# Kernel tuning notes

Hardware: AMD Instinct MI355X
Metric: run time of the kernel (lower is better)

The kernel has to match this reference:

```python
import jax, jax.numpy as jnp
import numpy as np

B, N, D, L = 8, 128, 512, 48
NUM_GCN_LAYERS = 2


def setup_inputs() -> dict:
    key = jax.random.key(0)
    ks = jax.random.split(key, 10)
    gcn_inputs = jax.random.normal(ks[0], (B, N, D), dtype=jnp.float32)
    word_seq_len = jax.random.randint(ks[1], (B,), 1, N + 1)
    adj_matrix = jax.random.randint(ks[2], (B, N, N), 0, 2).astype(jnp.float32)
    dep_label_matrix = jax.random.randint(ks[3], (B, N, N), 0, L)
    # per-label weight matrices, stored (L, out_dim, in_dim) as consumed by the bmm
    w_params = jax.random.normal(ks[4], (L, D, D), dtype=jnp.float32) * 0.05
    mlp_w0 = jax.random.normal(ks[5], (D, D), dtype=jnp.float32) * (1.0 / np.sqrt(D))
    mlp_b0 = jnp.zeros((D,), dtype=jnp.float32)
    mlp_w1 = jax.random.normal(ks[6], (D, D), dtype=jnp.float32) * (1.0 / np.sqrt(D))
    mlp_b1 = jnp.zeros((D,), dtype=jnp.float32)
    return {
        'gcn_inputs': gcn_inputs,
        'word_seq_len': word_seq_len,
        'adj_matrix': adj_matrix,
        'dep_label_matrix': dep_label_matrix,
        'w_params': w_params,
        'mlp_w0': mlp_w0,
        'mlp_b0': mlp_b0,
        'mlp_w1': mlp_w1,
        'mlp_b1': mlp_b1,
    }


def reference(gcn_inputs, word_seq_len, adj_matrix, dep_label_matrix,
              w_params, mlp_w0, mlp_b0, mlp_w1, mlp_b1):
    # denom: in-degree + 1 (self)
    denom = adj_matrix.sum(axis=2, keepdims=True) + 1.0  # (B, N, 1)
    b_idx = jnp.arange(B)[:, None, None]                  # (B,1,1)
    j_idx = jnp.arange(N)[None, None, :]                  # (1,1,N)
    h = gcn_inputs
    for _ in range(NUM_GCN_LAYERS):
        # transform every node by every label matrix: (B, L, N, D)
        t = jnp.einsum('ldk,bjk->bljd', w_params, h)
        # gather per-edge label transform: g[b,i,j,:] = t[b, lab[b,i,j], j, :]
        g = t[b_idx, dep_label_matrix, j_idx]             # (B, N, N, D)
        msg = (adj_matrix[..., None] * g).sum(axis=2)     # (B, N, D)
        h = jax.nn.relu(msg / denom)
    x = jax.nn.relu(h @ mlp_w0.T + mlp_b0)
    x = jax.nn.relu(x @ mlp_w1.T + mlp_b1)
    return x
```

## Files before the change

kernel.cpp:

```cpp
#include <hip/hip_runtime.h>
#include <hip/hip_bf16.h>


typedef unsigned short u16;
typedef unsigned int u32;
using bf16x8 = __bf16 __attribute__((ext_vector_type(8)));
using f32x4 = float __attribute__((ext_vector_type(4)));

__device__ __forceinline__ u16 f2bf(float f) {
  u32 u = __float_as_uint(f);
  u32 r = u + 0x7fffu + ((u >> 16) & 1u);
  return (u16)(r >> 16);
}
__device__ __forceinline__ float bf2f(u16 h) {
  return __uint_as_float(((u32)h) << 16);
}

__device__ __forceinline__ void gl_lds16(const u16* g, u16* l) {
  __builtin_amdgcn_global_load_lds(
      (const __attribute__((address_space(1))) u32*)g,
      (__attribute__((address_space(3))) u32*)l, 16, 0, 0);
}

__global__ __launch_bounds__(256)
void cvt_all(const float* __restrict__ w_in, u16* __restrict__ w_out,
             const float* __restrict__ h_in, u16* __restrict__ h_out,
             const float* __restrict__ w0, const float* __restrict__ w1,
             u16* __restrict__ Bp1, u16* __restrict__ Bp2) {
  const int bx = blockIdx.x;
  if (bx < 2048) {
    const int n4 = (48 * 512 * 512) / 4;
    const int stride = 2048 * 256;
    for (int i = bx * 256 + threadIdx.x; i < n4; i += stride) {
      float4 v = ((const float4*)w_in)[i];
      uint2 o;
      o.x = (u32)f2bf(v.x) | ((u32)f2bf(v.y) << 16);
      o.y = (u32)f2bf(v.z) | ((u32)f2bf(v.w) << 16);
      ((uint2*)w_out)[i] = o;
    }
  } else if (bx < 2560) {
    const int i = (bx - 2048) * 256 + threadIdx.x;
    float4 v = ((const float4*)h_in)[i];
    uint2 o;
    o.x = (u32)f2bf(v.x) | ((u32)f2bf(v.y) << 16);
    o.y = (u32)f2bf(v.z) | ((u32)f2bf(v.w) << 16);
    ((uint2*)h_out)[i] = o;
  } else {
    const int idx = (bx - 2560) * 256 + threadIdx.x;
    if (idx < 262144) {
      const int n = idx >> 9, k = idx & 511;
      const float v = w0[idx];
      const u16 hi = f2bf(v);
      const float lo = v - bf2f(hi);
      Bp1[n * 1024 + k] = hi;
      Bp1[n * 1024 + 512 + k] = f2bf(lo);
    } else {
      const int j = idx - 262144;
      const int n = j >> 9, k = j & 511;
      const float v = w1[j];
      const u16 hi = f2bf(v);
      const float lo = v - bf2f(hi);
      Bp2[n * 1536 + k] = hi;
      Bp2[n * 1536 + 512 + k] = f2bf(lo);
      Bp2[n * 1536 + 1024 + k] = hi;
    }
  }
}

#define BM 128
#define BN 128
#define BK 32

template <int MODE>
__global__ __launch_bounds__(256, 3)
void gemm_nt_bf16(const u16* __restrict__ A, const u16* __restrict__ B,
                  void* __restrict__ C, int N, int K, int KC, int AK) {
  __shared__ u16 sA[3][BM * BK];
  __shared__ u16 sB[3][BN * BK];
  const int tid = threadIdx.x;
  const int lane = tid & 63;
  const int wid = tid >> 6;
  const int wm = wid >> 1;
  const int wn = wid & 1;

  int m0, n0, kc;
  if (MODE == 0) {
    const int bid = blockIdx.x;
    const int xcd = bid & 7;
    const int r = bid >> 3;
    m0 = (r & 7) * BM;
    n0 = (xcd * 24 + (r >> 3)) * BN;
    kc = 0;
  } else {
    m0 = blockIdx.y * BM;
    n0 = blockIdx.x * BN;
    kc = blockIdx.z;
  }

  int acol;
  if (MODE == 0)      acol = 0;
  else if (MODE == 1) acol = (kc & 1) * 256;
  else                acol = (kc >> 2) * 512 + (kc & 1) * 256;

  const int srow = tid >> 2;
  const int scol = ((tid & 3) ^ ((tid >> 3) & 3)) * 8;
  const u16* gA0 = A + (size_t)(m0 + srow) * AK + acol + scol;
  const u16* gA1 = A + (size_t)(m0 + 64 + srow) * AK + acol + scol;
  const u16* gB0 = B + (size_t)(n0 + srow) * K + kc * KC + scol;
  const u16* gB1 = B + (size_t)(n0 + 64 + srow) * K + kc * KC + scol;

  auto stage = [&](int buf, int kt) {
    const int ko = kt * BK;
    gl_lds16(gA0 + ko, &sA[buf][tid * 8]);
    gl_lds16(gA1 + ko, &sA[buf][2048 + tid * 8]);
    gl_lds16(gB0 + ko, &sB[buf][tid * 8]);
    gl_lds16(gB1 + ko, &sB[buf][2048 + tid * 8]);
  };

  f32x4 acc[4][4];
#pragma unroll
  for (int i = 0; i < 4; ++i)
#pragma unroll
    for (int j = 0; j < 4; ++j)
      acc[i][j] = (f32x4){0.f, 0.f, 0.f, 0.f};

  const int NT = KC / BK;

  stage(0, 0);
  if (NT > 1) {
    stage(1, 1);
    asm volatile("s_waitcnt vmcnt(4)" ::: "memory");
  } else {
    asm volatile("s_waitcnt vmcnt(0)" ::: "memory");
  }
  __builtin_amdgcn_s_barrier();
  __builtin_amdgcn_sched_barrier(0);

  const int r15 = lane & 15;
  const int colswz = (((lane >> 4) ^ ((r15 >> 1) & 3))) * 8;
  for (int kt = 0; kt < NT; ++kt) {
    const int buf = kt % 3;
    if (kt + 2 < NT) stage((kt + 2) % 3, kt + 2);

    bf16x8 af[4], bfr[4];
#pragma unroll
    for (int mi = 0; mi < 4; ++mi)
      af[mi] = *(const bf16x8*)&sA[buf][(wm * 64 + mi * 16 + r15) * BK + colswz];
#pragma unroll
    for (int ni = 0; ni < 4; ++ni)
      bfr[ni] = *(const bf16x8*)&sB[buf][(wn * 64 + ni * 16 + r15) * BK + colswz];

#pragma unroll
    for (int mi = 0; mi < 4; ++mi)
#pragma unroll
      for (int ni = 0; ni < 4; ++ni)
        acc[mi][ni] = __builtin_amdgcn_mfma_f32_16x16x32_bf16(
            af[mi], bfr[ni], acc[mi][ni], 0, 0, 0);

    if (kt + 1 < NT) {
      if (kt + 2 < NT)
        asm volatile("s_waitcnt vmcnt(4)" ::: "memory");
      else
        asm volatile("s_waitcnt vmcnt(0)" ::: "memory");
      __builtin_amdgcn_s_barrier();
      __builtin_amdgcn_sched_barrier(0);
    }
  }

  const int rq = (lane >> 4) * 4;
#pragma unroll
  for (int mi = 0; mi < 4; ++mi) {
#pragma unroll
    for (int ni = 0; ni < 4; ++ni) {
      const int row = m0 + wm * 64 + mi * 16 + rq;
      const int col = n0 + wn * 64 + ni * 16 + r15;
      f32x4 v = acc[mi][ni];
      if (MODE == 0) {
        u16* Cb = (u16*)C;
        const size_t base = (size_t)row * N + col;
#pragma unroll
        for (int r = 0; r < 4; ++r)
          Cb[base + (size_t)r * N] = f2bf(v[r]);
      } else {
        float* Cf = (float*)C + (size_t)kc * 1024 * N;
#pragma unroll
        for (int r = 0; r < 4; ++r)
          Cf[(size_t)(row + r) * N + col] = v[r];
      }
    }
  }
}

__global__ __launch_bounds__(128)
void gcn_agg(const u16* __restrict__ T, const float* __restrict__ adj,
             const int* __restrict__ lab, u16* __restrict__ Hout) {
  const int bid = blockIdx.x;
  const int b = bid & 7;
  const int i = (bid >> 3) & 127;
  const int half = bid >> 10;
  const int bi = b * 128 + i;
  const int tid = threadIdx.x;
  __shared__ float s_adj[128];
  __shared__ int s_off[128];
  s_adj[tid] = adj[(size_t)bi * 128 + tid];
  s_off[tid] = ((b * 128 + tid) * 48 + lab[(size_t)bi * 128 + tid]) * 512;
  __syncthreads();

  const int d = half * 256 + tid * 2;
  float den = 1.0f, a0 = 0.f, a1 = 0.f;
#pragma unroll 4
  for (int j = 0; j < 128; ++j) {
    const float a = s_adj[j];
    if (a != 0.0f) {
      den += 1.0f;
      const u32 u = *(const u32*)&T[(size_t)s_off[j] + d];
      a0 += __uint_as_float((u & 0xffffu) << 16);
      a1 += __uint_as_float(u & 0xffff0000u);
    }
  }
  const float r = 1.0f / den;
  a0 = fmaxf(a0 * r, 0.0f);
  a1 = fmaxf(a1 * r, 0.0f);
  const u32 o = (u32)f2bf(a0) | ((u32)f2bf(a1) << 16);
  *(u32*)&Hout[(size_t)bi * 512 + d] = o;
}

__global__ __launch_bounds__(256)
void combine_mlp1(const float* __restrict__ P, const float* __restrict__ bias,
                  u16* __restrict__ X1) {
  const int idx = blockIdx.x * 256 + threadIdx.x;
  const int m = idx >> 8;
  const int n = (idx & 255) * 2;
  float s0 = 0.f, s1 = 0.f;
#pragma unroll
  for (int s = 0; s < 4; ++s) {
    const float2 v = *(const float2*)&P[(size_t)s * 524288 + m * 512 + n];
    s0 += v.x; s1 += v.y;
  }
  const float x0 = fmaxf(s0 + bias[n], 0.f);
  const float x1 = fmaxf(s1 + bias[n + 1], 0.f);
  const u16 h0 = f2bf(x0), h1 = f2bf(x1);
  const float l0 = x0 - bf2f(h0), l1 = x1 - bf2f(h1);
  const u32 hh = (u32)h0 | ((u32)h1 << 16);
  const u32 ll = (u32)f2bf(l0) | ((u32)f2bf(l1) << 16);
  const size_t base = (size_t)m * 1024 + n;
  *(u32*)&X1[base] = hh;
  *(u32*)&X1[base + 512] = ll;
}

__global__ __launch_bounds__(256)
void combine_mlp2(const float* __restrict__ P, const float* __restrict__ bias,
                  float* __restrict__ out) {
  const int idx = blockIdx.x * 256 + threadIdx.x;
  const int m = idx >> 7;
  const int n = (idx & 127) * 4;
  float4 s = {0.f, 0.f, 0.f, 0.f};
#pragma unroll
  for (int t = 0; t < 6; ++t) {
    const float4 v = *(const float4*)&P[(size_t)t * 524288 + m * 512 + n];
    s.x += v.x; s.y += v.y; s.z += v.z; s.w += v.w;
  }
  const float4 b = *(const float4*)&bias[n];
  float4 o;
  o.x = fmaxf(s.x + b.x, 0.f);
  o.y = fmaxf(s.y + b.y, 0.f);
  o.z = fmaxf(s.z + b.z, 0.f);
  o.w = fmaxf(s.w + b.w, 0.f);
  *(float4*)&out[(size_t)m * 512 + n] = o;
}

extern "C" void kernel_launch(void* const* d_in, const int* in_sizes, int n_in,
                              void* d_out, int out_size, void* d_ws, size_t ws_size,
                              hipStream_t stream) {
  const float* gcn_inputs = (const float*)d_in[0];
  const float* adj = (const float*)d_in[2];
  const int* lab = (const int*)d_in[3];
  const float* w_params = (const float*)d_in[4];
  const float* w0 = (const float*)d_in[5];
  const float* b0 = (const float*)d_in[6];
  const float* w1 = (const float*)d_in[7];
  const float* b1 = (const float*)d_in[8];
  float* out = (float*)d_out;

  char* ws = (char*)d_ws;
  u16* Wbf = (u16*)ws;
  float* P = (float*)ws;
  u16* T = (u16*)(ws + 25165824);
  u16* Ha = (u16*)(ws + 75497472);
  u16* Hb = (u16*)(ws + 76546048);
  u16* H2 = (u16*)(ws + 77594624);
  u16* X1 = (u16*)(ws + 79691776);
  u16* Bp1 = (u16*)(ws + 82837504);
  u16* Bp2 = (u16*)(ws + 83886080);

  cvt_all<<<4608, 256, 0, stream>>>(w_params, Wbf, gcn_inputs, Ha,
                                    w0, w1, Bp1, Bp2);

  gemm_nt_bf16<0><<<1536, 256, 0, stream>>>(Ha, Wbf, T, 24576, 512, 512, 512);
  gcn_agg<<<2048, 128, 0, stream>>>(T, adj, lab, Hb);
  gemm_nt_bf16<0><<<1536, 256, 0, stream>>>(Hb, Wbf, T, 24576, 512, 512, 512);
  gcn_agg<<<2048, 128, 0, stream>>>(T, adj, lab, H2);

  dim3 g1(512 / BN, 1024 / BM, 4);
  gemm_nt_bf16<1><<<g1, 256, 0, stream>>>(H2, Bp1, P, 512, 1024, 256, 512);
  combine_mlp1<<<1024, 256, 0, stream>>>(P, b0, X1);
  dim3 g2(512 / BN, 1024 / BM, 6);
  gemm_nt_bf16<2><<<g2, 256, 0, stream>>>(X1, Bp2, P, 512, 1536, 256, 1024);
  combine_mlp2<<<512, 256, 0, stream>>>(P, b1, out);
}
```

Measured before the change: 171.0 us.

## Replace split-K MLP GEMMs and combine kernels with fused 64x64 GEMM epilogue

```diff
diff --git a/kernel.cpp b/kernel.cpp
--- a/kernel.cpp
+++ b/kernel.cpp
@@ -191,22 +191,121 @@
   }
 }
 
-__global__ __launch_bounds__(128)
+template <int MODE>
+__global__ __launch_bounds__(256)
+void mlp_gemm64(const u16* __restrict__ A, const u16* __restrict__ B,
+                void* __restrict__ C, const float* __restrict__ bias) {
+  __shared__ u16 sA[3][64 * 32];
+  __shared__ u16 sB[3][64 * 32];
+  const int tid = threadIdx.x;
+  const int lane = tid & 63;
+  const int wid = tid >> 6;
+  const int wm = wid >> 1;
+  const int wn = wid & 1;
+  const int n0 = blockIdx.x * 64;
+  const int m0 = blockIdx.y * 64;
+  const int AK = (MODE == 1) ? 512 : 1024;
+  const int LDB = (MODE == 1) ? 1024 : 1536;
+  const int NT = (MODE == 1) ? 32 : 48;
+
+  const int srow = tid >> 2;
+  const int scol = ((tid & 3) ^ ((tid >> 3) & 3)) * 8;
+  const u16* gA = A + (size_t)(m0 + srow) * AK + scol;
+  const u16* gB = B + (size_t)(n0 + srow) * LDB + scol;
+
+  auto stage = [&](int buf, int kt) {
+    const int aoff = ((MODE == 2 && kt >= 32) ? 512 : 0) + (kt & 15) * 32;
+    gl_lds16(gA + aoff, &sA[buf][tid * 8]);
+    gl_lds16(gB + kt * 32, &sB[buf][tid * 8]);
+  };
+
+  f32x4 acc[2][2];
+#pragma unroll
+  for (int i = 0; i < 2; ++i)
+#pragma unroll
+    for (int j = 0; j < 2; ++j)
+      acc[i][j] = (f32x4){0.f, 0.f, 0.f, 0.f};
+
+  stage(0, 0);
+  stage(1, 1);
+  asm volatile("s_waitcnt vmcnt(2)" ::: "memory");
+  __builtin_amdgcn_s_barrier();
+  __builtin_amdgcn_sched_barrier(0);
+
+  const int r15 = lane & 15;
+  const int colswz = (((lane >> 4) ^ ((r15 >> 1) & 3))) * 8;
+  for (int kt = 0; kt < NT; ++kt) {
+    const int buf = kt % 3;
+    if (kt + 2 < NT) stage((kt + 2) % 3, kt + 2);
+
+    bf16x8 af[2], bfr[2];
+#pragma unroll
+    for (int mi = 0; mi < 2; ++mi)
+      af[mi] = *(const bf16x8*)&sA[buf][(wm * 32 + mi * 16 + r15) * 32 + colswz];
+#pragma unroll
+    for (int ni = 0; ni < 2; ++ni)
+      bfr[ni] = *(const bf16x8*)&sB[buf][(wn * 32 + ni * 16 + r15) * 32 + colswz];
+
+#pragma unroll
+    for (int mi = 0; mi < 2; ++mi)
+#pragma unroll
+      for (int ni = 0; ni < 2; ++ni)
+        acc[mi][ni] = __builtin_amdgcn_mfma_f32_16x16x32_bf16(
+            af[mi], bfr[ni], acc[mi][ni], 0, 0, 0);
+
+    if (kt + 1 < NT) {
+      if (kt + 2 < NT)
+        asm volatile("s_waitcnt vmcnt(2)" ::: "memory");
+      else
+        asm volatile("s_waitcnt vmcnt(0)" ::: "memory");
+      __builtin_amdgcn_s_barrier();
+      __builtin_amdgcn_sched_barrier(0);
+    }
+  }
+
+  const int rq = (lane >> 4) * 4;
+#pragma unroll
+  for (int mi = 0; mi < 2; ++mi) {
+#pragma unroll
+    for (int ni = 0; ni < 2; ++ni) {
+      const int row = m0 + wm * 32 + mi * 16 + rq;
+      const int col = n0 + wn * 32 + ni * 16 + r15;
+      const float bv = bias[col];
+      f32x4 v = acc[mi][ni];
+#pragma unroll
+      for (int r = 0; r < 4; ++r) {
+        const float x = fmaxf(v[r] + bv, 0.0f);
+        if (MODE == 1) {
+          u16* X1 = (u16*)C;
+          const u16 hi = f2bf(x);
+          const float lo = x - bf2f(hi);
+          X1[(size_t)(row + r) * 1024 + col] = hi;
+          X1[(size_t)(row + r) * 1024 + 512 + col] = f2bf(lo);
+        } else {
+          ((float*)C)[(size_t)(row + r) * 512 + col] = x;
+        }
+      }
+    }
+  }
+}
+
+__global__ __launch_bounds__(256)
 void gcn_agg(const u16* __restrict__ T, const float* __restrict__ adj,
              const int* __restrict__ lab, u16* __restrict__ Hout) {
   const int bid = blockIdx.x;
   const int b = bid & 7;
-  const int i = (bid >> 3) & 127;
-  const int half = bid >> 10;
+  const int i = bid >> 3;
   const int bi = b * 128 + i;
   const int tid = threadIdx.x;
   __shared__ float s_adj[128];
   __shared__ int s_off[128];
-  s_adj[tid] = adj[(size_t)bi * 128 + tid];
-  s_off[tid] = ((b * 128 + tid) * 48 + lab[(size_t)bi * 128 + tid]) * 512;
+  if (tid < 128) {
+    s_adj[tid] = adj[(size_t)bi * 128 + tid];
+    s_off[tid] = ((b * 128 + tid) * 48 + lab[(size_t)bi * 128 + tid]) * 512;
+  }
   __syncthreads();
 
-  const int d = half * 256 + tid * 2;
+  const int d = tid * 2;
   float den = 1.0f, a0 = 0.f, a1 = 0.f;
 #pragma unroll 4
   for (int j = 0; j < 128; ++j) {
@@ -223,50 +322,6 @@
   a1 = fmaxf(a1 * r, 0.0f);
   const u32 o = (u32)f2bf(a0) | ((u32)f2bf(a1) << 16);
   *(u32*)&Hout[(size_t)bi * 512 + d] = o;
-}
-
-__global__ __launch_bounds__(256)
-void combine_mlp1(const float* __restrict__ P, const float* __restrict__ bias,
-                  u16* __restrict__ X1) {
-  const int idx = blockIdx.x * 256 + threadIdx.x;
-  const int m = idx >> 8;
-  const int n = (idx & 255) * 2;
-  float s0 = 0.f, s1 = 0.f;
-#pragma unroll
-  for (int s = 0; s < 4; ++s) {
-    const float2 v = *(const float2*)&P[(size_t)s * 524288 + m * 512 + n];
-    s0 += v.x; s1 += v.y;
-  }
-  const float x0 = fmaxf(s0 + bias[n], 0.f);
-  const float x1 = fmaxf(s1 + bias[n + 1], 0.f);
-  const u16 h0 = f2bf(x0), h1 = f2bf(x1);
-  const float l0 = x0 - bf2f(h0), l1 = x1 - bf2f(h1);
-  const u32 hh = (u32)h0 | ((u32)h1 << 16);
-  const u32 ll = (u32)f2bf(l0) | ((u32)f2bf(l1) << 16);
-  const size_t base = (size_t)m * 1024 + n;
-  *(u32*)&X1[base] = hh;
-  *(u32*)&X1[base + 512] = ll;
-}
-
-__global__ __launch_bounds__(256)
-void combine_mlp2(const float* __restrict__ P, const float* __restrict__ bias,
-                  float* __restrict__ out) {
-  const int idx = blockIdx.x * 256 + threadIdx.x;
-  const int m = idx >> 7;
-  const int n = (idx & 127) * 4;
-  float4 s = {0.f, 0.f, 0.f, 0.f};
-#pragma unroll
-  for (int t = 0; t < 6; ++t) {
-    const float4 v = *(const float4*)&P[(size_t)t * 524288 + m * 512 + n];
-    s.x += v.x; s.y += v.y; s.z += v.z; s.w += v.w;
-  }
-  const float4 b = *(const float4*)&bias[n];
-  float4 o;
-  o.x = fmaxf(s.x + b.x, 0.f);
-  o.y = fmaxf(s.y + b.y, 0.f);
-  o.z = fmaxf(s.z + b.z, 0.f);
-  o.w = fmaxf(s.w + b.w, 0.f);
-  *(float4*)&out[(size_t)m * 512 + n] = o;
 }
 
 extern "C" void kernel_launch(void* const* d_in, const int* in_sizes, int n_in,
@@ -284,7 +339,6 @@
 
   char* ws = (char*)d_ws;
   u16* Wbf = (u16*)ws;
-  float* P = (float*)ws;
   u16* T = (u16*)(ws + 25165824);
   u16* Ha = (u16*)(ws + 75497472);
   u16* Hb = (u16*)(ws + 76546048);
@@ -297,14 +351,11 @@
                                     w0, w1, Bp1, Bp2);
 
   gemm_nt_bf16<0><<<1536, 256, 0, stream>>>(Ha, Wbf, T, 24576, 512, 512, 512);
-  gcn_agg<<<2048, 128, 0, stream>>>(T, adj, lab, Hb);
+  gcn_agg<<<1024, 256, 0, stream>>>(T, adj, lab, Hb);
   gemm_nt_bf16<0><<<1536, 256, 0, stream>>>(Hb, Wbf, T, 24576, 512, 512, 512);
-  gcn_agg<<<2048, 128, 0, stream>>>(T, adj, lab, H2);
-
-  dim3 g1(512 / BN, 1024 / BM, 4);
-  gemm_nt_bf16<1><<<g1, 256, 0, stream>>>(H2, Bp1, P, 512, 1024, 256, 512);
-  combine_mlp1<<<1024, 256, 0, stream>>>(P, b0, X1);
-  dim3 g2(512 / BN, 1024 / BM, 6);
-  gemm_nt_bf16<2><<<g2, 256, 0, stream>>>(X1, Bp2, P, 512, 1536, 256, 1024);
-  combine_mlp2<<<512, 256, 0, stream>>>(P, b1, out);
-}
+  gcn_agg<<<1024, 256, 0, stream>>>(T, adj, lab, H2);
+
+  dim3 gm(8, 16);
+  mlp_gemm64<1><<<gm, 256, 0, stream>>>(H2, Bp1, X1, b0);
+  mlp_gemm64<2><<<gm, 256, 0, stream>>>(X1, Bp2, out, b1);
+}
```

New measurement: 177.3 us. 1.04x slower.
